# Kernel tuning notes

Hardware: AMD Instinct MI355X
Metric: run time of the kernel (lower is better)

The kernel has to match this reference:

```python
import jax, jax.numpy as jnp
import numpy as np

VOCAB = 65
N_EMBED = 384
BLOCK = 256
N_HEAD = 6
HEAD_SIZE = 4  # forward uses sa_heads = MultiHeadAttention(4), NOT the Block stack
B, T = 128, 256


def setup_inputs() -> dict:
    key = jax.random.key(0)
    ks = jax.random.split(key, 16)
    s = lambda *sh: 0.02
    inp = {
        "idx": jax.random.randint(ks[0], (B, T), 0, VOCAB),
        "targets": jax.random.randint(ks[1], (B, T), 0, VOCAB),
        "tok_emb": jax.random.normal(ks[2], (VOCAB, N_EMBED), jnp.float32) * 0.02,
        "pos_emb": jax.random.normal(ks[3], (BLOCK, N_EMBED), jnp.float32) * 0.02,
        "Wq": jax.random.normal(ks[4], (N_HEAD, N_EMBED, HEAD_SIZE), jnp.float32) * 0.05,
        "Wk": jax.random.normal(ks[5], (N_HEAD, N_EMBED, HEAD_SIZE), jnp.float32) * 0.05,
        "Wv": jax.random.normal(ks[6], (N_HEAD, N_EMBED, HEAD_SIZE), jnp.float32) * 0.05,
        "Wproj": jax.random.normal(ks[7], (N_HEAD * HEAD_SIZE, N_EMBED), jnp.float32) * 0.05,
        "bproj": jnp.zeros((N_EMBED,), jnp.float32),
        "W1": jax.random.normal(ks[8], (N_EMBED, 4 * N_EMBED), jnp.float32) * 0.02,
        "b1": jnp.zeros((4 * N_EMBED,), jnp.float32),
        "W2": jax.random.normal(ks[9], (4 * N_EMBED, N_EMBED), jnp.float32) * 0.02,
        "b2": jnp.zeros((N_EMBED,), jnp.float32),
        "Wlm": jax.random.normal(ks[10], (N_EMBED, VOCAB), jnp.float32) * 0.02,
        "blm": jnp.zeros((VOCAB,), jnp.float32),
    }
    return inp


def _forward(idx, targets, tok_emb, pos_emb, Wq, Wk, Wv, Wproj, bproj, W1, b1, W2, b2, Wlm, blm):
    Bb, Tt = idx.shape
    x = tok_emb[idx] + pos_emb[:Tt]  # [B,T,C]
    # multi-head attention (manual, causal). NOTE: source scales by n_embed**-0.5 (C of input), not head_size.
    q = jnp.einsum("btc,hcd->bhtd", x, Wq)
    k = jnp.einsum("btc,hcd->bhtd", x, Wk)
    v = jnp.einsum("btc,hcd->bhtd", x, Wv)
    scores = jnp.einsum("bhtd,bhsd->bhts", q, k) * (N_EMBED ** -0.5)
    causal = jnp.tril(jnp.ones((Tt, Tt), bool))
    scores = jnp.where(causal, scores, -jnp.inf)
    w = jax.nn.softmax(scores, axis=-1)  # dropout = identity in eval
    attn = jnp.einsum("bhts,bhsd->bhtd", w, v)
    attn = attn.transpose(0, 2, 1, 3).reshape(Bb, Tt, N_HEAD * HEAD_SIZE)
    x = attn @ Wproj + bproj
    # feed-forward
    x = jax.nn.relu(x @ W1 + b1) @ W2 + b2
    logits = x @ Wlm + blm  # [B,T,V]
    logits_flat = logits.reshape(Bb * Tt, VOCAB)
    t_flat = targets.reshape(Bb * Tt)
    logp = jax.nn.log_softmax(logits_flat, axis=-1)
    loss = -jnp.mean(jnp.take_along_axis(logp, t_flat[:, None], axis=1))
    return logits_flat, loss


def reference(idx, targets, tok_emb, pos_emb, Wq, Wk, Wv, Wproj, bproj, W1, b1, W2, b2, Wlm, blm):
    return _forward(idx, targets, tok_emb, pos_emb, Wq, Wk, Wv, Wproj, bproj, W1, b1, W2, b2, Wlm, blm)
```

## Files before the change

### kernel.cpp

```cpp
#include <hip/hip_runtime.h>
#include <hip/hip_bf16.h>
#include <math.h>

typedef __hip_bfloat16 bf16;
typedef __attribute__((ext_vector_type(8))) short bf16x8;
typedef __attribute__((ext_vector_type(4))) float f32x4;
typedef __attribute__((ext_vector_type(8))) int i32x8;
typedef __attribute__((ext_vector_type(4))) int i32x4;
typedef unsigned char u8;
typedef unsigned int u32;

#define T_SEQ   256
#define C_EMB   384
#define NH      6
#define HS      4
#define NB      128
#define NTOK    (NB * T_SEQ)
#define VOC     65
#define FFDIM   1536
#define QKVW    72
#define PROJK   32
#define XROWS   (VOC * T_SEQ)

#define X2_SCALE    128.0f
#define W1_SCALE    128.0f
#define FF1_DESCALE (1.0f / (128.0f * 128.0f))
#define H1_SCALE    512.0f
#define W2_SCALE    128.0f
#define FF2_DESCALE (1.0f / (512.0f * 128.0f))

__device__ __forceinline__ float bf2f(bf16 x) { return __bfloat162float(x); }
__device__ __forceinline__ bf16  f2b(float x) { return __float2bfloat16(x); }
__device__ __forceinline__ short f2s(float x) { bf16 b = __float2bfloat16(x); return *reinterpret_cast<short*>(&b); }
__device__ __forceinline__ u8 f2fp8(float x) {
    return (u8)(__builtin_amdgcn_cvt_pk_fp8_f32(x, x, 0, false) & 0xff);
}
__device__ __forceinline__ u32 pk4fp8(const float* w) {
    int p = __builtin_amdgcn_cvt_pk_fp8_f32(w[0], w[1], 0, false);
    p = __builtin_amdgcn_cvt_pk_fp8_f32(w[2], w[3], p, true);
    return (u32)p;
}

__device__ __forceinline__ void glds16(const void* g, void* l) {
    __builtin_amdgcn_global_load_lds((const __attribute__((address_space(1))) void*)g,
                                     (__attribute__((address_space(3))) void*)l, 16, 0, 0);
}

__global__ void pack_all_kernel(const float* __restrict__ Wq, const float* __restrict__ Wk,
                                const float* __restrict__ Wv, const float* __restrict__ Wlm,
                                const float* __restrict__ Wproj,
                                const float* __restrict__ W1, const float* __restrict__ W2,
                                const float* __restrict__ tok_emb, const float* __restrict__ pos_emb,
                                bf16* __restrict__ WqkvT, bf16* __restrict__ WlmT,
                                bf16* __restrict__ WprojT, u8* __restrict__ W1f8,
                                u8* __restrict__ W2f8, bf16* __restrict__ xtab,
                                float* __restrict__ lossbuf) {
    int blk = blockIdx.x;
    if (blk == 0 && threadIdx.x == 0) { lossbuf[0] = 0.f; ((int*)lossbuf)[1] = 0; }
    if (blk < 128) {
        int n = blk;
        for (int c = threadIdx.x; c < C_EMB; c += 256) {
            float v = 0.f;
            if (n < QKVW) {
                int sel = n / 24, r = n % 24, h = r >> 2, d = r & 3;
                const float* W = (sel == 0) ? Wq : (sel == 1) ? Wk : Wv;
                v = W[(h * C_EMB + c) * HS + d];
            }
            WqkvT[(size_t)n * C_EMB + c] = f2b(v);
        }
    } else if (blk < 256) {
        int n = blk - 128;
        for (int c = threadIdx.x; c < C_EMB; c += 256)
            WlmT[(size_t)n * C_EMB + c] = f2b(n < VOC ? Wlm[(size_t)c * VOC + n] : 0.f);
    } else if (blk < 640) {
        int n = blk - 256;
        int k = threadIdx.x;
        if (k < PROJK)
            WprojT[(size_t)n * PROJK + k] = f2b(k < 24 ? Wproj[(size_t)k * C_EMB + n] : 0.f);
    } else if (blk < 640 + FFDIM) {
        int n = blk - 640;
        for (int k = threadIdx.x; k < C_EMB; k += 256)
            W1f8[(size_t)n * C_EMB + k] = f2fp8(W1[(size_t)k * FFDIM + n] * W1_SCALE);
    } else if (blk < 640 + FFDIM + C_EMB) {
        int n = blk - 640 - FFDIM;
        for (int k = threadIdx.x; k < FFDIM; k += 256)
            W2f8[(size_t)n * FFDIM + k] = f2fp8(W2[(size_t)k * C_EMB + n] * W2_SCALE);
    } else {
        int base = (blk - (640 + FFDIM + C_EMB)) * 4;
        for (int r = 0; r < 4; ++r) {
            int row = base + r;
            int id = row >> 8, t = row & 255;
            const float* te = tok_emb + (size_t)id * C_EMB;
            const float* pe = pos_emb + (size_t)t * C_EMB;
            bf16* dst = xtab + (size_t)row * C_EMB;
            for (int c = threadIdx.x; c < C_EMB; c += 256)
                dst[c] = f2b(te[c] + pe[c]);
        }
    }
}

__global__ __launch_bounds__(512)
void qkv_gather_kernel(const int* __restrict__ idx, const bf16* __restrict__ xtab,
                       const bf16* __restrict__ Bt, float* __restrict__ outf) {
    __shared__ __align__(16) u8 As[16384];
    __shared__ __align__(16) u8 Bs[16384];
    __shared__ int rowid[128];
    int tid = threadIdx.x, lane = tid & 63, wave = tid >> 6;
    int bm = blockIdx.x * 128;
    int wm = (wave & 1) * 64, wn = (wave >> 1) * 32;
    int lrow = lane & 15, kq = lane >> 4;
    if (tid < 128) { int token = bm + tid; rowid[tid] = idx[token] * T_SEQ + (token & (T_SEQ - 1)); }
    __syncthreads();

    int r0 = tid >> 3;
    int s0 = (((tid & 7) * 16) - (r0 & 7) * 16) & 127;
    int c1 = tid + 512;
    int r1 = c1 >> 3;
    int s1 = (((c1 & 7) * 16) - (r1 & 7) * 16) & 127;
    const u8* xb = (const u8*)xtab;
    const u8* bb = (const u8*)Bt;
    long gA0 = (long)rowid[r0] * 768 + s0;
    long gA1 = (long)rowid[r1] * 768 + s1;
    long gB0 = (long)r0 * 768 + s0;
    long gB1 = (long)r1 * 768 + s1;
    int ro = (lrow & 7) * 16;

    f32x4 acc[4][2] = {};
    for (int k0 = 0; k0 < 768; k0 += 128) {
        glds16(xb + gA0 + k0, As + (size_t)tid * 16);
        glds16(xb + gA1 + k0, As + (size_t)c1 * 16);
        glds16(bb + gB0 + k0, Bs + (size_t)tid * 16);
        glds16(bb + gB1 + k0, Bs + (size_t)c1 * 16);
        __syncthreads();
        #pragma unroll
        for (int ks = 0; ks < 2; ++ks) {
            int off = (ks * 64 + kq * 16 + ro) & 127;
            bf16x8 af[4], bff[2];
            #pragma unroll
            for (int i = 0; i < 4; ++i)
                af[i] = *(const bf16x8*)&As[(size_t)(wm + i * 16 + lrow) * 128 + off];
            #pragma unroll
            for (int i = 0; i < 2; ++i)
                bff[i] = *(const bf16x8*)&Bs[(size_t)(wn + i * 16 + lrow) * 128 + off];
            #pragma unroll
            for (int mi = 0; mi < 4; ++mi)
                #pragma unroll
                for (int ni = 0; ni < 2; ++ni)
                    acc[mi][ni] = __builtin_amdgcn_mfma_f32_16x16x32_bf16(af[mi], bff[ni], acc[mi][ni], 0, 0, 0);
        }
        __syncthreads();
    }

    #pragma unroll
    for (int ni = 0; ni < 2; ++ni) {
        int col = wn + ni * 16 + lrow;
        if (col >= QKVW) continue;
        #pragma unroll
        for (int mi = 0; mi < 4; ++mi) {
            int orow = bm + wm + mi * 16 + kq * 4;
            #pragma unroll
            for (int r = 0; r < 4; ++r)
                outf[(size_t)(orow + r) * QKVW + col] = acc[mi][ni][r];
        }
    }
}

__global__ void attn_kernel(const float* __restrict__ qkv,
                            bf16* __restrict__ attnT) {
    int bh = blockIdx.x;
    int b = bh / NH, h = bh % NH;
    int t = threadIdx.x;
    __shared__ float4 kv[T_SEQ][2];
    const float* base = qkv + (size_t)(b * T_SEQ) * QKVW;
    kv[t][0] = *(const float4*)(base + t * QKVW + 24 + h * HS);
    kv[t][1] = *(const float4*)(base + t * QKVW + 48 + h * HS);
    __syncthreads();
    const float scale = 0.05103103630798288f;
    float4 q = *(const float4*)(base + t * QKVW + h * HS);
    float qx = q.x * scale, qy = q.y * scale, qz = q.z * scale, qw = q.w * scale;
    float sum0 = 0.f, sum1 = 0.f;
    float o0x = 0.f, o0y = 0.f, o0z = 0.f, o0w = 0.f;
    float o1x = 0.f, o1y = 0.f, o1z = 0.f, o1w = 0.f;
    int s = 0;
    for (; s + 1 <= t; s += 2) {
        float4 k0 = kv[s][0],     v0 = kv[s][1];
        float4 k1 = kv[s + 1][0], v1 = kv[s + 1][1];
        float p0 = __expf(qx * k0.x + qy * k0.y + qz * k0.z + qw * k0.w);
        float p1 = __expf(qx * k1.x + qy * k1.y + qz * k1.z + qw * k1.w);
        sum0 += p0; sum1 += p1;
        o0x += p0 * v0.x; o0y += p0 * v0.y; o0z += p0 * v0.z; o0w += p0 * v0.w;
        o1x += p1 * v1.x; o1y += p1 * v1.y; o1z += p1 * v1.z; o1w += p1 * v1.w;
    }
    if (s <= t) {
        float4 k0 = kv[s][0], v0 = kv[s][1];
        float p0 = __expf(qx * k0.x + qy * k0.y + qz * k0.z + qw * k0.w);
        sum0 += p0;
        o0x += p0 * v0.x; o0y += p0 * v0.y; o0z += p0 * v0.z; o0w += p0 * v0.w;
    }
    float inv = 1.f / (sum0 + sum1);
    bf16* out = attnT + (size_t)(b * T_SEQ + t) * PROJK + h * HS;
    out[0] = f2b((o0x + o1x) * inv);
    out[1] = f2b((o0y + o1y) * inv);
    out[2] = f2b((o0z + o1z) * inv);
    out[3] = f2b((o0w + o1w) * inv);
    if (h == 0) {
        bf16* pad = attnT + (size_t)(b * T_SEQ + t) * PROJK + 24;
        *(uint4*)pad = uint4{0, 0, 0, 0};
    }
}

__global__ __launch_bounds__(512, 2)
void ff_mega_kernel(const bf16* __restrict__ attnT, const bf16* __restrict__ WprojT,
                    const float* __restrict__ bproj,
                    const u8* __restrict__ W1f8, const float* __restrict__ b1,
                    const u8* __restrict__ W2f8, const float* __restrict__ b2,
                    bf16* __restrict__ x3) {
    __shared__ __align__(16) u8 smem[147456];
    u8* x2_lds = smem;
    u8* bs1    = smem + 49152;
    u8* h1t    = smem + 114688;
    short* As_p = (short*)(smem + 49152);
    short* Bs_p = (short*)(smem + 57344);

    int tid  = threadIdx.x;
    int lane = tid & 63;
    int wave = tid >> 6;
    int bm   = blockIdx.x * 128;
    int lrow  = lane & 15;
    int khalf = lane >> 4;
    int wm  = (wave & 1) * 64;
    int wn6 = (wave >> 1) * 96;
    int wn4 = (wave >> 1) * 64;

    {
        int row = tid >> 2;
        int i0 = (tid & 3) * 16;
        int selem = ((i0 - ((row >> 1) & 3) * 16) & 63) >> 1;
        glds16(attnT + (size_t)(bm + row) * PROJK + selem, As_p + (size_t)tid * 8);
        #pragma unroll
        for (int p = 0; p < 3; ++p) {
            int c = tid + p * 512;
            int rowb = c >> 2;
            int sel2 = (((c & 3) * 16 - ((rowb >> 1) & 3) * 16) & 63) >> 1;
            glds16(WprojT + (size_t)rowb * PROJK + sel2, Bs_p + (size_t)c * 8);
        }
    }
    __syncthreads();

    f32x4 accp[4][6] = {};
    {
        int arot16 = ((lrow >> 1) & 3) * 16;
        int roff = ((khalf * 16 + arot16) & 63) >> 1;
        bf16x8 afp[4], bfp[6];
        #pragma unroll
        for (int i = 0; i < 4; ++i)
            afp[i] = *(const bf16x8*)&As_p[(size_t)(wm + i * 16 + lrow) * 32 + roff];
        #pragma unroll
        for (int i = 0; i < 6; ++i)
            bfp[i] = *(const bf16x8*)&Bs_p[(size_t)(wn6 + i * 16 + lrow) * 32 + roff];
        #pragma unroll
        for (int mi = 0; mi < 4; ++mi)
            #pragma unroll
            for (int ni = 0; ni < 6; ++ni)
                accp[mi][ni] = __builtin_amdgcn_mfma_f32_16x16x32_bf16(bfp[ni], afp[mi], accp[mi][ni], 0, 0, 0);
    }
    __syncthreads();

    #pragma unroll
    for (int p = 0; p < 4; ++p) {
        int c = tid + p * 512;
        int row = c >> 3;
        int sr = (((c & 7) * 16) - (row & 7) * 16) & 127;
        glds16(W1f8 + (size_t)row * 384 + sr, bs1 + (size_t)c * 16);
    }

    #pragma unroll
    for (int mi = 0; mi < 4; ++mi) {
        int m = wm + mi * 16 + lrow;
        #pragma unroll
        for (int ni = 0; ni < 6; ++ni) {
            int n0 = wn6 + ni * 16 + khalf * 4;
            float4 bv = *(const float4*)(bproj + n0);
            float w[4];
            w[0] = (accp[mi][ni][0] + bv.x) * X2_SCALE;
            w[1] = (accp[mi][ni][1] + bv.y) * X2_SCALE;
            w[2] = (accp[mi][ni][2] + bv.z) * X2_SCALE;
            w[3] = (accp[mi][ni][3] + bv.w) * X2_SCALE;
            *(u32*)&x2_lds[(size_t)(n0 >> 7) * 16384 + (size_t)m * 128 +
                           (((n0 & 127) + (m & 7) * 16) & 127)] = pk4fp8(w);
        }
    }
    __syncthreads();

    int arot8 = (lrow & 7) * 16;
    int off0 = (khalf * 32 + arot8) & 127;
    int off1 = (off0 + 16) & 127;

    f32x4 acc1[4][4] = {};
    f32x4 acc2[4][6] = {};

    for (int nt = 0; nt < 6; ++nt) {
        #pragma unroll
        for (int kk = 0; kk < 3; ++kk) {
            int stp = nt * 3 + kk;
            if (stp + 1 < 18) {
                int nnt = (stp + 1) / 3, nk0 = ((stp + 1) % 3) * 128;
                u8* dst = bs1 + (size_t)((stp + 1) & 1) * 32768;
                #pragma unroll
                for (int p = 0; p < 4; ++p) {
                    int c = tid + p * 512;
                    int row = c >> 3;
                    int sr = (((c & 7) * 16) - (row & 7) * 16) & 127;
                    glds16(W1f8 + (size_t)(nnt * 256 + row) * 384 + nk0 + sr,
                           dst + (size_t)c * 16);
                }
            }
            const u8* abase = x2_lds + (size_t)kk * 16384;
            const u8* bbase = bs1 + (size_t)(stp & 1) * 32768;
            i32x8 a[4];
            #pragma unroll
            for (int i = 0; i < 4; ++i) {
                const u8* rp = abase + (size_t)(wm + i * 16 + lrow) * 128;
                i32x4 lo = *(const i32x4*)(rp + off0);
                i32x4 hi = *(const i32x4*)(rp + off1);
                a[i][0]=lo[0]; a[i][1]=lo[1]; a[i][2]=lo[2]; a[i][3]=lo[3];
                a[i][4]=hi[0]; a[i][5]=hi[1]; a[i][6]=hi[2]; a[i][7]=hi[3];
            }
            #pragma unroll
            for (int nh = 0; nh < 2; ++nh) {
                i32x8 b[2];
                #pragma unroll
                for (int j = 0; j < 2; ++j) {
                    int ni = nh * 2 + j;
                    const u8* rp = bbase + (size_t)(wn4 + ni * 16 + lrow) * 128;
                    i32x4 lo = *(const i32x4*)(rp + off0);
                    i32x4 hi = *(const i32x4*)(rp + off1);
                    b[j][0]=lo[0]; b[j][1]=lo[1]; b[j][2]=lo[2]; b[j][3]=lo[3];
                    b[j][4]=hi[0]; b[j][5]=hi[1]; b[j][6]=hi[2]; b[j][7]=hi[3];
                }
                #pragma unroll
                for (int mi = 0; mi < 4; ++mi)
                    #pragma unroll
                    for (int j = 0; j < 2; ++j)
                        acc1[mi][nh * 2 + j] = __builtin_amdgcn_mfma_scale_f32_16x16x128_f8f6f4(
                            b[j], a[mi], acc1[mi][nh * 2 + j], 0, 0,
                            0, 0x7f7f7f7f, 0, 0x7f7f7f7f);
            }
            __syncthreads();
        }

        #pragma unroll
        for (int mi = 0; mi < 4; ++mi) {
            int m = wm + mi * 16 + lrow;
            #pragma unroll
            for (int ni = 0; ni < 4; ++ni) {
                int n0 = wn4 + ni * 16 + khalf * 4;
                float4 bv = *(const float4*)(b1 + nt * 256 + n0);
                float w[4];
                w[0] = fmaxf(acc1[mi][ni][0] * FF1_DESCALE + bv.x, 0.f) * H1_SCALE;
                w[1] = fmaxf(acc1[mi][ni][1] * FF1_DESCALE + bv.y, 0.f) * H1_SCALE;
                w[2] = fmaxf(acc1[mi][ni][2] * FF1_DESCALE + bv.z, 0.f) * H1_SCALE;
                w[3] = fmaxf(acc1[mi][ni][3] * FF1_DESCALE + bv.w, 0.f) * H1_SCALE;
                *(u32*)&h1t[(size_t)m * 256 + ((n0 + (m & 7) * 16) & 255)] = pk4fp8(w);
                acc1[mi][ni] = f32x4{0.f, 0.f, 0.f, 0.f};
            }
        }
        __syncthreads();

        #pragma unroll
        for (int sk = 0; sk < 2; ++sk) {
            i32x8 a2[4];
            #pragma unroll
            for (int i = 0; i < 4; ++i) {
                const u8* rp = h1t + (size_t)(wm + i * 16 + lrow) * 256;
                int o0 = (sk * 128 + khalf * 32 + arot8) & 255;
                int o1 = (sk * 128 + khalf * 32 + 16 + arot8) & 255;
                i32x4 lo = *(const i32x4*)(rp + o0);
                i32x4 hi = *(const i32x4*)(rp + o1);
                a2[i][0]=lo[0]; a2[i][1]=lo[1]; a2[i][2]=lo[2]; a2[i][3]=lo[3];
                a2[i][4]=hi[0]; a2[i][5]=hi[1]; a2[i][6]=hi[2]; a2[i][7]=hi[3];
            }
            #pragma unroll
            for (int half = 0; half < 2; ++half) {
                i32x8 bw[3];
                #pragma unroll
                for (int j = 0; j < 3; ++j) {
                    int n = wn6 + (half * 3 + j) * 16 + lrow;
                    const u8* p = W2f8 + (size_t)n * 1536 + nt * 256 + sk * 128 + khalf * 32;
                    i32x4 lo = *(const i32x4*)p;
                    i32x4 hi = *(const i32x4*)(p + 16);
                    bw[j][0]=lo[0]; bw[j][1]=lo[1]; bw[j][2]=lo[2]; bw[j][3]=lo[3];
                    bw[j][4]=hi[0]; bw[j][5]=hi[1]; bw[j][6]=hi[2]; bw[j][7]=hi[3];
                }
                #pragma unroll
                for (int mi = 0; mi < 4; ++mi)
                    #pragma unroll
                    for (int j = 0; j < 3; ++j)
                        acc2[mi][half * 3 + j] = __builtin_amdgcn_mfma_scale_f32_16x16x128_f8f6f4(
                            bw[j], a2[mi], acc2[mi][half * 3 + j], 0, 0,
                            0, 0x7f7f7f7f, 0, 0x7f7f7f7f);
            }
        }
        __syncthreads();
    }

    u8* Ep = smem;
    #pragma unroll
    for (int mi = 0; mi < 4; ++mi) {
        int m = wm + mi * 16 + lrow;
        #pragma unroll
        for (int ni = 0; ni < 6; ++ni) {
            int n0 = wn6 + ni * 16 + khalf * 4;
            float4 bv = *(const float4*)(b2 + n0);
            union { short s[4]; uint2 u; } pk;
            pk.s[0] = f2s(acc2[mi][ni][0] * FF2_DESCALE + bv.x);
            pk.s[1] = f2s(acc2[mi][ni][1] * FF2_DESCALE + bv.y);
            pk.s[2] = f2s(acc2[mi][ni][2] * FF2_DESCALE + bv.z);
            pk.s[3] = f2s(acc2[mi][ni][3] * FF2_DESCALE + bv.w);
            *(uint2*)&Ep[(size_t)m * 768 + ((n0 >> 7) << 8) +
                         ((((n0 & 127) * 2) + (m & 7) * 16) & 255)] = pk.u;
        }
    }
    __syncthreads();
    #pragma unroll
    for (int p = 0; p < 12; ++p) {
        int c = tid + p * 512;
        int row = c / 48;
        int sl = c - row * 48;
        int g0 = sl * 16;
        int chunk = g0 >> 8;
        int loc = g0 & 255;
        uint4 v = *(const uint4*)&Ep[(size_t)row * 768 + (chunk << 8) +
                                     ((loc + (row & 7) * 16) & 255)];
        *(uint4*)((u8*)x3 + (size_t)(bm + row) * 768 + g0) = v;
    }
}

__global__ __launch_bounds__(512)
void lm_loss_kernel(const bf16* __restrict__ A, const bf16* __restrict__ Bt,
                    const float* __restrict__ bias, const int* __restrict__ targets,
                    float* __restrict__ outf, float* __restrict__ lossbuf,
                    float* __restrict__ out_loss, int M, int K) {
    __shared__ short As[128][32];
    __shared__ short Bs[128][32];
    __shared__ float Ls[128][66];
    __shared__ float red[128];
    int tid  = threadIdx.x;
    int lane = tid & 63;
    int wave = tid >> 6;
    int bm = blockIdx.x * 128;
    int wm = (wave & 1) * 64;
    int wn = (wave >> 1) * 32;
    int lrow  = lane & 15;
    int khalf = lane >> 4;

    int row = tid >> 2;
    int i0 = (tid & 3) * 16;
    int selem = ((i0 - ((row >> 1) & 3) * 16) & 63) >> 1;
    int arot = ((lrow >> 1) & 3) * 16;
    int roff = ((khalf * 16 + arot) & 63) >> 1;

    f32x4 acc[4][2] = {};
    for (int k0 = 0; k0 < K; k0 += 32) {
        glds16(A  + (size_t)(bm + row) * K + k0 + selem, (short*)As + (size_t)tid * 8);
        glds16(Bt + (size_t)row * K + k0 + selem,        (short*)Bs + (size_t)tid * 8);
        __syncthreads();

        bf16x8 af[4], bff[2];
        #pragma unroll
        for (int i = 0; i < 4; ++i)
            af[i] = *(const bf16x8*)&As[wm + i * 16 + lrow][roff];
        #pragma unroll
        for (int i = 0; i < 2; ++i)
            bff[i] = *(const bf16x8*)&Bs[wn + i * 16 + lrow][roff];
        #pragma unroll
        for (int mi = 0; mi < 4; ++mi)
            #pragma unroll
            for (int ni = 0; ni < 2; ++ni)
                acc[mi][ni] = __builtin_amdgcn_mfma_f32_16x16x32_bf16(af[mi], bff[ni], acc[mi][ni], 0, 0, 0);
        __syncthreads();
    }

    #pragma unroll
    for (int ni = 0; ni < 2; ++ni) {
        int col = wn + ni * 16 + lrow;
        if (col >= VOC) continue;
        float bv = bias[col];
        #pragma unroll
        for (int mi = 0; mi < 4; ++mi) {
            int lr = wm + mi * 16 + khalf * 4;
            #pragma unroll
            for (int r = 0; r < 4; ++r) {
                float v = acc[mi][ni][r] + bv;
                outf[(size_t)(bm + lr + r) * VOC + col] = v;
                Ls[lr + r][col] = v;
            }
        }
    }
    __syncthreads();

    if (tid < 128) {
        int token = bm + tid;
        int tgt = targets[token];
        float m = -1e30f, s = 0.f;
        #pragma unroll 8
        for (int c = 0; c < VOC; ++c) {
            float v = Ls[tid][c];
            float mn = fmaxf(m, v);
            s = s * __expf(m - mn) + __expf(v - mn);
            m = mn;
        }
        red[tid] = m + logf(s) - Ls[tid][tgt];
    }
    __syncthreads();
    if (tid < 64) {
        float s = red[tid] + red[tid + 64];
        #pragma unroll
        for (int off = 32; off > 0; off >>= 1) s += __shfl_xor(s, off);
        if (tid == 0) {
            atomicAdd(&lossbuf[0], s);
            __threadfence();
            int done = atomicAdd(&((int*)lossbuf)[1], 1);
            if (done == (NTOK / 128) - 1) {
                __threadfence();
                float total = atomicAdd(&lossbuf[0], 0.0f);
                out_loss[0] = total / (float)NTOK;
            }
        }
    }
}

extern "C" void kernel_launch(void* const* d_in, const int* in_sizes, int n_in,
                              void* d_out, int out_size, void* d_ws, size_t ws_size,
                              hipStream_t stream) {
    const int*   idx     = (const int*)  d_in[0];
    const int*   targets = (const int*)  d_in[1];
    const float* tok_emb = (const float*)d_in[2];
    const float* pos_emb = (const float*)d_in[3];
    const float* Wq      = (const float*)d_in[4];
    const float* Wk      = (const float*)d_in[5];
    const float* Wv      = (const float*)d_in[6];
    const float* Wproj   = (const float*)d_in[7];
    const float* bproj   = (const float*)d_in[8];
    const float* W1      = (const float*)d_in[9];
    const float* b1      = (const float*)d_in[10];
    const float* W2      = (const float*)d_in[11];
    const float* b2      = (const float*)d_in[12];
    const float* Wlm     = (const float*)d_in[13];
    const float* blm     = (const float*)d_in[14];

    char* ws = (char*)d_ws;
    bf16*  WprojT = (bf16*) (ws + 0);
    float* qkvbuf = (float*)(ws + 25165824);
    bf16*  attnT  = (bf16*) (ws + 34603008);
    bf16*  xtab   = (bf16*) (ws + 37748736);
    bf16*  x3     = (bf16*) (ws + 163577856);
    float* lossbuf= (float*)(ws + 188743680);
    u8*    W1f8   = (u8*)   (ws + 188874752);
    u8*    W2f8   = (u8*)   (ws + 190054400);
    bf16*  WqkvT  = (bf16*) (ws + 191234048);
    bf16*  WlmT   = (bf16*) (ws + 191332352);

    float* out_logits = (float*)d_out;
    float* out_loss   = out_logits + (size_t)NTOK * VOC;

    pack_all_kernel<<<640 + FFDIM + C_EMB + XROWS / 4, 256, 0, stream>>>(
        Wq, Wk, Wv, Wlm, Wproj, W1, W2, tok_emb, pos_emb,
        WqkvT, WlmT, WprojT, W1f8, W2f8, xtab, lossbuf);

    qkv_gather_kernel<<<NTOK / 128, 512, 0, stream>>>(idx, xtab, WqkvT, qkvbuf);
    attn_kernel<<<NB * NH, T_SEQ, 0, stream>>>(qkvbuf, attnT);

    ff_mega_kernel<<<NTOK / 128, 512, 0, stream>>>(attnT, WprojT, bproj,
                                                   W1f8, b1, W2f8, b2, x3);

    lm_loss_kernel<<<NTOK / 128, 512, 0, stream>>>(x3, WlmT, blm, targets,
                                                   out_logits, lossbuf, out_loss, NTOK, C_EMB);
}
```

Before: 247.2 us.

## Pre-pack FP8 FFN weights in MFMA fragment order and load W1 directly from global

The pack kernel now writes W1 and W2 as FP8 in per-lane MFMA fragment order (2 KB tiles of 16 rows by 128 K), so each lane reads 32 contiguous bytes. The FF mega kernel drops the double-buffered LDS staging of W1 and its per-step barriers, loading B fragments straight from global/L2, and shrinks LDS from 144 KB to 96 KB. This removes LDS traffic and synchronisation in the first FFN GEMM and may allow higher occupancy. In exchange, every wave re-reads the weights from L2 with exposed global latency instead of sharing one LDS copy per block.

```diff
diff --git a/kernel.cpp b/kernel.cpp
--- a/kernel.cpp
+++ b/kernel.cpp
@@ -52,14 +52,15 @@
                                 const float* __restrict__ W1, const float* __restrict__ W2,
                                 const float* __restrict__ tok_emb, const float* __restrict__ pos_emb,
                                 bf16* __restrict__ WqkvT, bf16* __restrict__ WlmT,
-                                bf16* __restrict__ WprojT, u8* __restrict__ W1f8,
-                                u8* __restrict__ W2f8, bf16* __restrict__ xtab,
+                                bf16* __restrict__ WprojT, u8* __restrict__ W1P,
+                                u8* __restrict__ W2P, bf16* __restrict__ xtab,
                                 float* __restrict__ lossbuf) {
     int blk = blockIdx.x;
-    if (blk == 0 && threadIdx.x == 0) { lossbuf[0] = 0.f; ((int*)lossbuf)[1] = 0; }
+    int t = threadIdx.x;
+    if (blk == 0 && t == 0) { lossbuf[0] = 0.f; ((int*)lossbuf)[1] = 0; }
     if (blk < 128) {
         int n = blk;
-        for (int c = threadIdx.x; c < C_EMB; c += 256) {
+        for (int c = t; c < C_EMB; c += 256) {
             float v = 0.f;
             if (n < QKVW) {
                 int sel = n / 24, r = n % 24, h = r >> 2, d = r & 3;
@@ -70,30 +71,48 @@
         }
     } else if (blk < 256) {
         int n = blk - 128;
-        for (int c = threadIdx.x; c < C_EMB; c += 256)
+        for (int c = t; c < C_EMB; c += 256)
             WlmT[(size_t)n * C_EMB + c] = f2b(n < VOC ? Wlm[(size_t)c * VOC + n] : 0.f);
     } else if (blk < 640) {
         int n = blk - 256;
-        int k = threadIdx.x;
+        int k = t;
         if (k < PROJK)
             WprojT[(size_t)n * PROJK + k] = f2b(k < 24 ? Wproj[(size_t)k * C_EMB + n] : 0.f);
-    } else if (blk < 640 + FFDIM) {
-        int n = blk - 640;
-        for (int k = threadIdx.x; k < C_EMB; k += 256)
-            W1f8[(size_t)n * C_EMB + k] = f2fp8(W1[(size_t)k * FFDIM + n] * W1_SCALE);
-    } else if (blk < 640 + FFDIM + C_EMB) {
-        int n = blk - 640 - FFDIM;
-        for (int k = threadIdx.x; k < FFDIM; k += 256)
-            W2f8[(size_t)n * FFDIM + k] = f2fp8(W2[(size_t)k * C_EMB + n] * W2_SCALE);
+    } else if (blk < 640 + 288) {
+        int fb = blk - 640;
+        int n16 = fb / 3, kk = fb % 3;
+        int b0 = t * 8;
+        int l = b0 >> 5;
+        int j0 = b0 & 31;
+        int n = n16 * 16 + (l & 15);
+        int kb = kk * 128 + (l >> 4) * 32 + j0;
+        union { u8 b[8]; uint2 u; } pk;
+        #pragma unroll
+        for (int e = 0; e < 8; ++e)
+            pk.b[e] = f2fp8(W1[(size_t)(kb + e) * FFDIM + n] * W1_SCALE);
+        *(uint2*)&W1P[(size_t)fb * 2048 + b0] = pk.u;
+    } else if (blk < 640 + 576) {
+        int fb = blk - 640 - 288;
+        int n16 = fb / 12, kc = fb % 12;
+        int b0 = t * 8;
+        int l = b0 >> 5;
+        int j0 = b0 & 31;
+        int n = n16 * 16 + (l & 15);
+        int kb = kc * 128 + (l >> 4) * 32 + j0;
+        union { u8 b[8]; uint2 u; } pk;
+        #pragma unroll
+        for (int e = 0; e < 8; ++e)
+            pk.b[e] = f2fp8(W2[(size_t)(kb + e) * C_EMB + n] * W2_SCALE);
+        *(uint2*)&W2P[(size_t)fb * 2048 + b0] = pk.u;
     } else {
-        int base = (blk - (640 + FFDIM + C_EMB)) * 4;
+        int base = (blk - (640 + 576)) * 4;
         for (int r = 0; r < 4; ++r) {
             int row = base + r;
-            int id = row >> 8, t = row & 255;
+            int id = row >> 8, tt = row & 255;
             const float* te = tok_emb + (size_t)id * C_EMB;
-            const float* pe = pos_emb + (size_t)t * C_EMB;
+            const float* pe = pos_emb + (size_t)tt * C_EMB;
             bf16* dst = xtab + (size_t)row * C_EMB;
-            for (int c = threadIdx.x; c < C_EMB; c += 256)
+            for (int c = t; c < C_EMB; c += 256)
                 dst[c] = f2b(te[c] + pe[c]);
         }
     }
@@ -212,13 +231,12 @@
 __global__ __launch_bounds__(512, 2)
 void ff_mega_kernel(const bf16* __restrict__ attnT, const bf16* __restrict__ WprojT,
                     const float* __restrict__ bproj,
-                    const u8* __restrict__ W1f8, const float* __restrict__ b1,
-                    const u8* __restrict__ W2f8, const float* __restrict__ b2,
+                    const u8* __restrict__ W1P, const float* __restrict__ b1,
+                    const u8* __restrict__ W2P, const float* __restrict__ b2,
                     bf16* __restrict__ x3) {
-    __shared__ __align__(16) u8 smem[147456];
+    __shared__ __align__(16) u8 smem[98304];
     u8* x2_lds = smem;
-    u8* bs1    = smem + 49152;
-    u8* h1t    = smem + 114688;
+    u8* h1t    = smem + 49152;
     short* As_p = (short*)(smem + 49152);
     short* Bs_p = (short*)(smem + 57344);
 
@@ -263,15 +281,6 @@
             #pragma unroll
             for (int ni = 0; ni < 6; ++ni)
                 accp[mi][ni] = __builtin_amdgcn_mfma_f32_16x16x32_bf16(bfp[ni], afp[mi], accp[mi][ni], 0, 0, 0);
-    }
-    __syncthreads();
-
-    #pragma unroll
-    for (int p = 0; p < 4; ++p) {
-        int c = tid + p * 512;
-        int row = c >> 3;
-        int sr = (((c & 7) * 16) - (row & 7) * 16) & 127;
-        glds16(W1f8 + (size_t)row * 384 + sr, bs1 + (size_t)c * 16);
     }
 
     #pragma unroll
@@ -302,21 +311,7 @@
     for (int nt = 0; nt < 6; ++nt) {
         #pragma unroll
         for (int kk = 0; kk < 3; ++kk) {
-            int stp = nt * 3 + kk;
-            if (stp + 1 < 18) {
-                int nnt = (stp + 1) / 3, nk0 = ((stp + 1) % 3) * 128;
-                u8* dst = bs1 + (size_t)((stp + 1) & 1) * 32768;
-                #pragma unroll
-                for (int p = 0; p < 4; ++p) {
-                    int c = tid + p * 512;
-                    int row = c >> 3;
-                    int sr = (((c & 7) * 16) - (row & 7) * 16) & 127;
-                    glds16(W1f8 + (size_t)(nnt * 256 + row) * 384 + nk0 + sr,
-                           dst + (size_t)c * 16);
-                }
-            }
             const u8* abase = x2_lds + (size_t)kk * 16384;
-            const u8* bbase = bs1 + (size_t)(stp & 1) * 32768;
             i32x8 a[4];
             #pragma unroll
             for (int i = 0; i < 4; ++i) {
@@ -326,27 +321,24 @@
                 a[i][0]=lo[0]; a[i][1]=lo[1]; a[i][2]=lo[2]; a[i][3]=lo[3];
                 a[i][4]=hi[0]; a[i][5]=hi[1]; a[i][6]=hi[2]; a[i][7]=hi[3];
             }
-            #pragma unroll
-            for (int nh = 0; nh < 2; ++nh) {
-                i32x8 b[2];
+            const u8* wbase = W1P + ((size_t)((nt * 16 + (wave >> 1) * 4) * 3 + kk)) * 2048
+                                  + (size_t)lane * 32;
+            i32x8 b[4];
+            #pragma unroll
+            for (int j = 0; j < 4; ++j) {
+                const u8* p = wbase + (size_t)j * 3 * 2048;
+                i32x4 lo = *(const i32x4*)p;
+                i32x4 hi = *(const i32x4*)(p + 16);
+                b[j][0]=lo[0]; b[j][1]=lo[1]; b[j][2]=lo[2]; b[j][3]=lo[3];
+                b[j][4]=hi[0]; b[j][5]=hi[1]; b[j][6]=hi[2]; b[j][7]=hi[3];
+            }
+            #pragma unroll
+            for (int mi = 0; mi < 4; ++mi)
                 #pragma unroll
-                for (int j = 0; j < 2; ++j) {
-                    int ni = nh * 2 + j;
-                    const u8* rp = bbase + (size_t)(wn4 + ni * 16 + lrow) * 128;
-                    i32x4 lo = *(const i32x4*)(rp + off0);
-                    i32x4 hi = *(const i32x4*)(rp + off1);
-                    b[j][0]=lo[0]; b[j][1]=lo[1]; b[j][2]=lo[2]; b[j][3]=lo[3];
-                    b[j][4]=hi[0]; b[j][5]=hi[1]; b[j][6]=hi[2]; b[j][7]=hi[3];
-                }
-                #pragma unroll
-                for (int mi = 0; mi < 4; ++mi)
-                    #pragma unroll
-                    for (int j = 0; j < 2; ++j)
-                        acc1[mi][nh * 2 + j] = __builtin_amdgcn_mfma_scale_f32_16x16x128_f8f6f4(
-                            b[j], a[mi], acc1[mi][nh * 2 + j], 0, 0,
-                            0, 0x7f7f7f7f, 0, 0x7f7f7f7f);
-            }
-            __syncthreads();
+                for (int j = 0; j < 4; ++j)
+                    acc1[mi][j] = __builtin_amdgcn_mfma_scale_f32_16x16x128_f8f6f4(
+                        b[j], a[mi], acc1[mi][j], 0, 0,
+                        0, 0x7f7f7f7f, 0, 0x7f7f7f7f);
         }
 
         #pragma unroll
@@ -380,13 +372,14 @@
                 a2[i][0]=lo[0]; a2[i][1]=lo[1]; a2[i][2]=lo[2]; a2[i][3]=lo[3];
                 a2[i][4]=hi[0]; a2[i][5]=hi[1]; a2[i][6]=hi[2]; a2[i][7]=hi[3];
             }
+            int kc = nt * 2 + sk;
             #pragma unroll
             for (int half = 0; half < 2; ++half) {
                 i32x8 bw[3];
                 #pragma unroll
                 for (int j = 0; j < 3; ++j) {
-                    int n = wn6 + (half * 3 + j) * 16 + lrow;
-                    const u8* p = W2f8 + (size_t)n * 1536 + nt * 256 + sk * 128 + khalf * 32;
+                    int n16 = (wave >> 1) * 6 + half * 3 + j;
+                    const u8* p = W2P + ((size_t)n16 * 12 + kc) * 2048 + (size_t)lane * 32;
                     i32x4 lo = *(const i32x4*)p;
                     i32x4 hi = *(const i32x4*)(p + 16);
                     bw[j][0]=lo[0]; bw[j][1]=lo[1]; bw[j][2]=lo[2]; bw[j][3]=lo[3];
@@ -556,23 +549,23 @@
     bf16*  xtab   = (bf16*) (ws + 37748736);
     bf16*  x3     = (bf16*) (ws + 163577856);
     float* lossbuf= (float*)(ws + 188743680);
-    u8*    W1f8   = (u8*)   (ws + 188874752);
-    u8*    W2f8   = (u8*)   (ws + 190054400);
+    u8*    W1P    = (u8*)   (ws + 188874752);
+    u8*    W2P    = (u8*)   (ws + 190054400);
     bf16*  WqkvT  = (bf16*) (ws + 191234048);
     bf16*  WlmT   = (bf16*) (ws + 191332352);
 
     float* out_logits = (float*)d_out;
     float* out_loss   = out_logits + (size_t)NTOK * VOC;
 
-    pack_all_kernel<<<640 + FFDIM + C_EMB + XROWS / 4, 256, 0, stream>>>(
+    pack_all_kernel<<<640 + 576 + XROWS / 4, 256, 0, stream>>>(
         Wq, Wk, Wv, Wlm, Wproj, W1, W2, tok_emb, pos_emb,
-        WqkvT, WlmT, WprojT, W1f8, W2f8, xtab, lossbuf);
+        WqkvT, WlmT, WprojT, W1P, W2P, xtab, lossbuf);
 
     qkv_gather_kernel<<<NTOK / 128, 512, 0, stream>>>(idx, xtab, WqkvT, qkvbuf);
     attn_kernel<<<NB * NH, T_SEQ, 0, stream>>>(qkvbuf, attnT);
 
     ff_mega_kernel<<<NTOK / 128, 512, 0, stream>>>(attnT, WprojT, bproj,
-                                                   W1f8, b1, W2f8, b2, x3);
+                                                   W1P, b1, W2P, b2, x3);
 
     lm_loss_kernel<<<NTOK / 128, 512, 0, stream>>>(x3, WlmT, blm, targets,
                                                    out_logits, lossbuf, out_loss, NTOK, C_EMB);
```

Result: faster. 214.1 us (-13.4%).
